# Optimization experiments

Hardware: AMD Instinct MI355X
Metric: run time of the kernel (lower is better)

The kernel has to match this reference:

```python
import jax, jax.numpy as jnp
import numpy as np

N = 50000   # nodes
E = 800000  # edges (avg in-degree 16)
H = 4       # attention heads
F = 64      # in/out feats per head
NEG_SLOPE = 0.2  # DGL GATConv default


def setup_inputs() -> dict:
    key = jax.random.key(0)
    ks = jax.random.split(key, 12)
    s = 0.1
    x = jax.random.normal(ks[0], (N, F), jnp.float32)
    src = jax.random.randint(ks[1], (E,), 0, N, jnp.int32)
    dst = jax.random.randint(ks[2], (E,), 0, N, jnp.int32)
    W1 = (jax.random.normal(ks[3], (F, H * F), jnp.float32) * s)
    al1 = (jax.random.normal(ks[4], (H, F), jnp.float32) * s)
    ar1 = (jax.random.normal(ks[5], (H, F), jnp.float32) * s)
    b1 = jnp.zeros((H, F), jnp.float32)
    W2 = (jax.random.normal(ks[6], (F, H * F), jnp.float32) * s)
    al2 = (jax.random.normal(ks[7], (H, F), jnp.float32) * s)
    ar2 = (jax.random.normal(ks[8], (H, F), jnp.float32) * s)
    b2 = jnp.zeros((H, F), jnp.float32)
    return dict(x=x, src=src, dst=dst, W1=W1, al1=al1, ar1=ar1, b1=b1,
                W2=W2, al2=al2, ar2=ar2, b2=b2)


def _gat_layer(x, src, dst, W, al, ar, b):
    # Linear projection, split into heads: [N, H, F]
    h = (x @ W).reshape(N, H, F)
    # Per-node attention logits: [N, H]
    el = jnp.einsum('nhf,hf->nh', h, al)
    er = jnp.einsum('nhf,hf->nh', h, ar)
    # Per-edge score, LeakyReLU: [E, H]
    e = jax.nn.leaky_relu(el[src] + er[dst], NEG_SLOPE)
    # Edge-softmax over incoming edges of each dst node (segment softmax)
    emax = jax.ops.segment_max(e, dst, num_segments=N)        # [N, H]
    ee = jnp.exp(e - emax[dst])                               # [E, H]
    denom = jax.ops.segment_sum(ee, dst, num_segments=N)      # [N, H]
    alpha = ee / denom[dst]                                   # [E, H]
    # Weighted aggregation: gather src feats, scale, scatter-add to dst
    m = h[src] * alpha[..., None]                              # [E, H, F]
    out = jax.ops.segment_sum(m, dst, num_segments=N)          # [N, H, F]
    return out + b[None]


def reference(x, src, dst, W1, al1, ar1, b1, W2, al2, ar2, b2):
    # Layer 1: GATConv with tanh activation, then head-mean
    h = _gat_layer(x, src, dst, W1, al1, ar1, b1)
    h = jnp.tanh(h).mean(axis=-2)              # [N, F]
    # Layer 2: GATConv (no activation), then head-mean
    h = _gat_layer(h, src, dst, W2, al2, ar2, b2)
    return h.mean(axis=-2)                     # [N, F]
```

## Files before the change

### kernel.cpp

```cpp
#include <hip/hip_runtime.h>
#include <hip/hip_fp16.h>
#include <cfloat>
#include <cstddef>

#define NODES 50000
#define EDGES 800000
#define HEADS 4
#define FEAT  64
#define HF    256
#define NEG_SLOPE 0.2f


__global__ void zero_deg_kernel(int* __restrict__ deg) {
  int i = blockIdx.x * blockDim.x + threadIdx.x;
  if (i < NODES) deg[i] = 0;
}

__global__ void count_deg_kernel(const int* __restrict__ dst, int* __restrict__ deg) {
  int e = blockIdx.x * blockDim.x + threadIdx.x;
  if (e < EDGES) atomicAdd(&deg[dst[e]], 1);
}

__global__ __launch_bounds__(1024) void scan_kernel(const int* __restrict__ deg,
                                                    int* __restrict__ rowstart,
                                                    int* __restrict__ cursor) {
  __shared__ int wtot[16], wexcl[16];
  __shared__ int carry_s;
  const int tid = threadIdx.x, lane = tid & 63, wv = tid >> 6;
  if (tid == 0) carry_s = 0;
  __syncthreads();
  for (int base = 0; base < NODES; base += 4096) {
    const int i0 = base + tid * 4;
    int v0 = (i0 + 0 < NODES) ? deg[i0 + 0] : 0;
    int v1 = (i0 + 1 < NODES) ? deg[i0 + 1] : 0;
    int v2 = (i0 + 2 < NODES) ? deg[i0 + 2] : 0;
    int v3 = (i0 + 3 < NODES) ? deg[i0 + 3] : 0;
    const int t = v0 + v1 + v2 + v3;
    int x = t;
#pragma unroll
    for (int off = 1; off < 64; off <<= 1) {
      int u = __shfl_up(x, off, 64);
      if (lane >= off) x += u;
    }
    if (lane == 63) wtot[wv] = x;
    __syncthreads();
    if (wv == 0) {
      int wval = (lane < 16) ? wtot[lane] : 0;
      int wx = wval;
#pragma unroll
      for (int off = 1; off < 16; off <<= 1) {
        int u = __shfl_up(wx, off, 64);
        if (lane >= off) wx += u;
      }
      if (lane < 16) wexcl[lane] = wx - wval;
    }
    __syncthreads();
    const int carry = carry_s;
    int e = carry + wexcl[wv] + (x - t);
    if (i0 + 0 < NODES) { rowstart[i0 + 0] = e; cursor[i0 + 0] = e; } e += v0;
    if (i0 + 1 < NODES) { rowstart[i0 + 1] = e; cursor[i0 + 1] = e; } e += v1;
    if (i0 + 2 < NODES) { rowstart[i0 + 2] = e; cursor[i0 + 2] = e; } e += v2;
    if (i0 + 3 < NODES) { rowstart[i0 + 3] = e; cursor[i0 + 3] = e; }
    __syncthreads();
    if (tid == 1023) carry_s = carry + wexcl[15] + wtot[15];
    __syncthreads();
  }
}

__global__ void scatter_kernel(const int* __restrict__ src, const int* __restrict__ dst,
                               int* __restrict__ cursor, int* __restrict__ csr_src) {
  int e = blockIdx.x * blockDim.x + threadIdx.x;
  if (e < EDGES) {
    int pos = atomicAdd(&cursor[dst[e]], 1);
    csr_src[pos] = src[e];
  }
}

template<int ROWS>
__global__ __launch_bounds__(256) void proj_kernel(
    const float* __restrict__ x, const float* __restrict__ W,
    const float* __restrict__ al, const float* __restrict__ ar,
    __half* __restrict__ h, float* __restrict__ el, float* __restrict__ er) {
  __shared__ float xs[ROWS * FEAT];
  const int c = threadIdx.x;
  const int head = c >> 6, f = c & 63;

  float Wc[FEAT];
#pragma unroll
  for (int k = 0; k < FEAT; ++k) Wc[k] = W[k * HF + c];
  const float alv = al[head * FEAT + f];
  const float arv = ar[head * FEAT + f];

  const int row0 = blockIdx.x * ROWS;
  for (int i = c; i < ROWS * FEAT; i += 256) {
    int r = row0 + (i >> 6);
    xs[i] = (r < NODES) ? x[r * FEAT + (i & 63)] : 0.f;
  }
  __syncthreads();

  for (int r = 0; r < ROWS; ++r) {
    const int row = row0 + r;
    if (row >= NODES) break;
    const float4* xr = (const float4*)&xs[r * FEAT];
    float v = 0.f;
#pragma unroll
    for (int k4 = 0; k4 < 16; ++k4) {
      float4 xv = xr[k4];
      v += xv.x * Wc[4 * k4 + 0] + xv.y * Wc[4 * k4 + 1] +
           xv.z * Wc[4 * k4 + 2] + xv.w * Wc[4 * k4 + 3];
    }
    h[(size_t)row * HF + c] = __float2half(v);
    float sl = v * alv, sr = v * arv;
#pragma unroll
    for (int m = 32; m; m >>= 1) {
      sl += __shfl_xor(sl, m, 64);
      sr += __shfl_xor(sr, m, 64);
    }
    if (f == 0) {
      el[row * HEADS + head] = sl;
      er[row * HEADS + head] = sr;
    }
  }
}

__device__ __forceinline__ float lrelu(float s) { return s > 0.f ? s : NEG_SLOPE * s; }

__device__ __forceinline__ void gather_fma(const __half* __restrict__ h, int s,
                                           int hh, int fq, float av, float4& acc) {
  union { uint2 u; __half2 h2[2]; } cvt;
  cvt.u = *(const uint2*)(h + (size_t)s * HF + hh * FEAT + fq * 4);
  float2 f01 = __half22float2(cvt.h2[0]);
  float2 f23 = __half22float2(cvt.h2[1]);
  acc.x += f01.x * av;
  acc.y += f01.y * av;
  acc.z += f23.x * av;
  acc.w += f23.y * av;
}

template<int DO_TANH>
__global__ __launch_bounds__(256) void node_kernel(
    const int* __restrict__ rowstart, const int* __restrict__ deg,
    const int* __restrict__ csr_src,
    const float* __restrict__ el, const float* __restrict__ er,
    const __half* __restrict__ h, const float* __restrict__ bias,
    float* __restrict__ out) {
  const int node = (blockIdx.x * blockDim.x + threadIdx.x) >> 6;
  if (node >= NODES) return;
  const int lane = threadIdx.x & 63;
  const int hh = lane >> 4, fq = lane & 15;
  const int rs = rowstart[node];
  const int dg = deg[node];

  float4 acc = make_float4(0.f, 0.f, 0.f, 0.f);

  if (dg > 0) {
    const float4 erv = *(const float4*)&er[node * 4];
    if (dg <= 64) {
      int sL = 0;
      float s0 = -FLT_MAX, s1 = -FLT_MAX, s2 = -FLT_MAX, s3 = -FLT_MAX;
      if (lane < dg) {
        sL = csr_src[rs + lane];
        float4 ev = *(const float4*)&el[sL * 4];
        s0 = lrelu(ev.x + erv.x);
        s1 = lrelu(ev.y + erv.y);
        s2 = lrelu(ev.z + erv.z);
        s3 = lrelu(ev.w + erv.w);
      }
      float m0 = s0, m1 = s1, m2 = s2, m3 = s3;
#pragma unroll
      for (int off = 32; off; off >>= 1) {
        m0 = fmaxf(m0, __shfl_xor(m0, off, 64));
        m1 = fmaxf(m1, __shfl_xor(m1, off, 64));
        m2 = fmaxf(m2, __shfl_xor(m2, off, 64));
        m3 = fmaxf(m3, __shfl_xor(m3, off, 64));
      }
      float E0 = 0.f, E1 = 0.f, E2 = 0.f, E3 = 0.f;
      if (lane < dg) {
        E0 = __expf(s0 - m0);
        E1 = __expf(s1 - m1);
        E2 = __expf(s2 - m2);
        E3 = __expf(s3 - m3);
      }
      float q0 = E0, q1 = E1, q2 = E2, q3 = E3;
#pragma unroll
      for (int off = 32; off; off >>= 1) {
        q0 += __shfl_xor(q0, off, 64);
        q1 += __shfl_xor(q1, off, 64);
        q2 += __shfl_xor(q2, off, 64);
        q3 += __shfl_xor(q3, off, 64);
      }
      const float A0 = E0 / q0, A1 = E1 / q1, A2 = E2 / q2, A3 = E3 / q3;
      for (int i = 0; i < dg; ++i) {
        const int s = __shfl(sL, i, 64);
        const float a0 = __shfl(A0, i, 64);
        const float a1 = __shfl(A1, i, 64);
        const float a2 = __shfl(A2, i, 64);
        const float a3 = __shfl(A3, i, 64);
        const float av = (hh == 0) ? a0 : (hh == 1) ? a1 : (hh == 2) ? a2 : a3;
        gather_fma(h, s, hh, fq, av, acc);
      }
    } else {
      float m0 = -FLT_MAX, m1 = -FLT_MAX, m2 = -FLT_MAX, m3 = -FLT_MAX;
      for (int i = lane; i < dg; i += 64) {
        int s = csr_src[rs + i];
        float4 ev = *(const float4*)&el[s * 4];
        m0 = fmaxf(m0, lrelu(ev.x + erv.x));
        m1 = fmaxf(m1, lrelu(ev.y + erv.y));
        m2 = fmaxf(m2, lrelu(ev.z + erv.z));
        m3 = fmaxf(m3, lrelu(ev.w + erv.w));
      }
#pragma unroll
      for (int off = 32; off; off >>= 1) {
        m0 = fmaxf(m0, __shfl_xor(m0, off, 64));
        m1 = fmaxf(m1, __shfl_xor(m1, off, 64));
        m2 = fmaxf(m2, __shfl_xor(m2, off, 64));
        m3 = fmaxf(m3, __shfl_xor(m3, off, 64));
      }
      float q0 = 0.f, q1 = 0.f, q2 = 0.f, q3 = 0.f;
      for (int i = lane; i < dg; i += 64) {
        int s = csr_src[rs + i];
        float4 ev = *(const float4*)&el[s * 4];
        q0 += __expf(lrelu(ev.x + erv.x) - m0);
        q1 += __expf(lrelu(ev.y + erv.y) - m1);
        q2 += __expf(lrelu(ev.z + erv.z) - m2);
        q3 += __expf(lrelu(ev.w + erv.w) - m3);
      }
#pragma unroll
      for (int off = 32; off; off >>= 1) {
        q0 += __shfl_xor(q0, off, 64);
        q1 += __shfl_xor(q1, off, 64);
        q2 += __shfl_xor(q2, off, 64);
        q3 += __shfl_xor(q3, off, 64);
      }
      const float r0 = 1.f / q0, r1 = 1.f / q1, r2 = 1.f / q2, r3 = 1.f / q3;
      for (int base = 0; base < dg; base += 64) {
        const int cnt = min(64, dg - base);
        int sL = 0;
        float A0 = 0.f, A1 = 0.f, A2 = 0.f, A3 = 0.f;
        if (base + lane < dg) {
          sL = csr_src[rs + base + lane];
          float4 ev = *(const float4*)&el[sL * 4];
          A0 = __expf(lrelu(ev.x + erv.x) - m0) * r0;
          A1 = __expf(lrelu(ev.y + erv.y) - m1) * r1;
          A2 = __expf(lrelu(ev.z + erv.z) - m2) * r2;
          A3 = __expf(lrelu(ev.w + erv.w) - m3) * r3;
        }
        for (int i = 0; i < cnt; ++i) {
          const int s = __shfl(sL, i, 64);
          const float a0 = __shfl(A0, i, 64);
          const float a1 = __shfl(A1, i, 64);
          const float a2 = __shfl(A2, i, 64);
          const float a3 = __shfl(A3, i, 64);
          const float av = (hh == 0) ? a0 : (hh == 1) ? a1 : (hh == 2) ? a2 : a3;
          gather_fma(h, s, hh, fq, av, acc);
        }
      }
    }
  }

  const float4 bv = *(const float4*)&bias[hh * FEAT + fq * 4];
  float vx = acc.x + bv.x, vy = acc.y + bv.y, vz = acc.z + bv.z, vw = acc.w + bv.w;
  if (DO_TANH) { vx = tanhf(vx); vy = tanhf(vy); vz = tanhf(vz); vw = tanhf(vw); }
#pragma unroll
  for (int off = 16; off <= 32; off <<= 1) {
    vx += __shfl_xor(vx, off, 64);
    vy += __shfl_xor(vy, off, 64);
    vz += __shfl_xor(vz, off, 64);
    vw += __shfl_xor(vw, off, 64);
  }
  if (hh == 0) {
    *(float4*)&out[(size_t)node * FEAT + fq * 4] =
        make_float4(vx * 0.25f, vy * 0.25f, vz * 0.25f, vw * 0.25f);
  }
}


extern "C" void kernel_launch(void* const* d_in, const int* in_sizes, int n_in,
                              void* d_out, int out_size, void* d_ws, size_t ws_size,
                              hipStream_t stream) {
  const float* x   = (const float*)d_in[0];
  const int*   src = (const int*)d_in[1];
  const int*   dst = (const int*)d_in[2];
  const float* Ws[2]  = {(const float*)d_in[3], (const float*)d_in[7]};
  const float* als[2] = {(const float*)d_in[4], (const float*)d_in[8]};
  const float* ars[2] = {(const float*)d_in[5], (const float*)d_in[9]};
  const float* bs[2]  = {(const float*)d_in[6], (const float*)d_in[10]};

  float* ws = (float*)d_ws;
  const size_t NHF = (size_t)NODES * HF;
  const size_t NF  = (size_t)NODES * FEAT;
  const size_t NH  = (size_t)NODES * HEADS;
  __half* hbuf = (__half*)ws;
  float* x2   = ws + NHF / 2;
  float* el   = x2 + NF;
  float* er   = el + NH;
  int* ibase   = (int*)(er + NH);
  int* deg      = ibase;
  int* rowstart = ibase + NODES;
  int* cursor   = ibase + 2 * NODES;
  int* csr_src  = ibase + 3 * NODES;
  float* outp = (float*)d_out;

  const int ROWS = 32;
  const int proj_grid = (NODES + ROWS - 1) / ROWS;
  const int edge_grid = (EDGES + 255) / 256;
  const int node_grid = (NODES * 64) / 256;
  const int n_grid    = (NODES + 255) / 256;

  zero_deg_kernel<<<n_grid, 256, 0, stream>>>(deg);
  count_deg_kernel<<<edge_grid, 256, 0, stream>>>(dst, deg);
  scan_kernel<<<1, 1024, 0, stream>>>(deg, rowstart, cursor);
  scatter_kernel<<<edge_grid, 256, 0, stream>>>(src, dst, cursor, csr_src);

  proj_kernel<ROWS><<<proj_grid, 256, 0, stream>>>(x, Ws[0], als[0], ars[0], hbuf, el, er);
  node_kernel<1><<<node_grid, 256, 0, stream>>>(rowstart, deg, csr_src, el, er,
                                                hbuf, bs[0], x2);
  proj_kernel<ROWS><<<proj_grid, 256, 0, stream>>>(x2, Ws[1], als[1], ars[1], hbuf, el, er);
  node_kernel<0><<<node_grid, 256, 0, stream>>>(rowstart, deg, csr_src, el, er,
                                                hbuf, bs[1], outp);
}
```

Before: 492.3 us.

## Fuse degree counting into layer-1 projection and stage scan through shared memory

Folds the edge in-degree atomic counting into the first projection kernel as extra blocks. This removes one launch and lets the counting overlap with the projection GEMM. The single-block scan now loads 13312-element chunks into LDS, with each thread doing a serial scan over 13 elements, which cuts the number of loop iterations and barriers. The projection dot product is also split into four independent accumulators to shorten the FMA dependency chain. The costs are a larger LDS footprint in the scan and mixed work types inside one grid.

```diff
diff --git a/kernel.cpp b/kernel.cpp
--- a/kernel.cpp
+++ b/kernel.cpp
@@ -10,59 +10,71 @@
 #define HF    256
 #define NEG_SLOPE 0.2f
 
+#define ROWS 32
+#define PROJ_BLOCKS ((NODES + ROWS - 1) / ROWS)
+#define COUNT_BLOCKS ((EDGES + 255) / 256)
+
 
 __global__ void zero_deg_kernel(int* __restrict__ deg) {
   int i = blockIdx.x * blockDim.x + threadIdx.x;
   if (i < NODES) deg[i] = 0;
 }
 
-__global__ void count_deg_kernel(const int* __restrict__ dst, int* __restrict__ deg) {
-  int e = blockIdx.x * blockDim.x + threadIdx.x;
-  if (e < EDGES) atomicAdd(&deg[dst[e]], 1);
-}
-
+#define SCHUNK 13312
+#define SPER   13
 __global__ __launch_bounds__(1024) void scan_kernel(const int* __restrict__ deg,
                                                     int* __restrict__ rowstart,
                                                     int* __restrict__ cursor) {
-  __shared__ int wtot[16], wexcl[16];
+  __shared__ int buf[SCHUNK];
+  __shared__ int wsum[16];
   __shared__ int carry_s;
   const int tid = threadIdx.x, lane = tid & 63, wv = tid >> 6;
   if (tid == 0) carry_s = 0;
-  __syncthreads();
-  for (int base = 0; base < NODES; base += 4096) {
-    const int i0 = base + tid * 4;
-    int v0 = (i0 + 0 < NODES) ? deg[i0 + 0] : 0;
-    int v1 = (i0 + 1 < NODES) ? deg[i0 + 1] : 0;
-    int v2 = (i0 + 2 < NODES) ? deg[i0 + 2] : 0;
-    int v3 = (i0 + 3 < NODES) ? deg[i0 + 3] : 0;
-    const int t = v0 + v1 + v2 + v3;
-    int x = t;
+  for (int base = 0; base < NODES; base += SCHUNK) {
+    const int sz = min(SCHUNK, NODES - base);
+    for (int i = tid; i < sz; i += 1024) buf[i] = deg[base + i];
+    __syncthreads();
+    const int o = tid * SPER;
+    int tsum = 0;
+#pragma unroll
+    for (int j = 0; j < SPER; ++j) {
+      int idx = o + j;
+      if (idx < sz) tsum += buf[idx];
+    }
+    int x = tsum;
 #pragma unroll
     for (int off = 1; off < 64; off <<= 1) {
       int u = __shfl_up(x, off, 64);
       if (lane >= off) x += u;
     }
-    if (lane == 63) wtot[wv] = x;
+    if (lane == 63) wsum[wv] = x;
     __syncthreads();
     if (wv == 0) {
-      int wval = (lane < 16) ? wtot[lane] : 0;
+      int wval = (lane < 16) ? wsum[lane] : 0;
       int wx = wval;
 #pragma unroll
       for (int off = 1; off < 16; off <<= 1) {
         int u = __shfl_up(wx, off, 64);
         if (lane >= off) wx += u;
       }
-      if (lane < 16) wexcl[lane] = wx - wval;
+      if (lane < 16) wsum[lane] = wx - wval;
     }
     __syncthreads();
     const int carry = carry_s;
-    int e = carry + wexcl[wv] + (x - t);
-    if (i0 + 0 < NODES) { rowstart[i0 + 0] = e; cursor[i0 + 0] = e; } e += v0;
-    if (i0 + 1 < NODES) { rowstart[i0 + 1] = e; cursor[i0 + 1] = e; } e += v1;
-    if (i0 + 2 < NODES) { rowstart[i0 + 2] = e; cursor[i0 + 2] = e; } e += v2;
-    if (i0 + 3 < NODES) { rowstart[i0 + 3] = e; cursor[i0 + 3] = e; }
-    __syncthreads();
-    if (tid == 1023) carry_s = carry + wexcl[15] + wtot[15];
+    int run = carry + wsum[wv] + (x - tsum);
+#pragma unroll
+    for (int j = 0; j < SPER; ++j) {
+      int idx = o + j;
+      if (idx < sz) { int t = buf[idx]; buf[idx] = run; run += t; }
+    }
+    __syncthreads();
+    for (int i = tid; i < sz; i += 1024) {
+      int v = buf[i];
+      rowstart[base + i] = v;
+      cursor[base + i] = v;
+    }
+    __syncthreads();
+    if (tid == 1023) carry_s = run;
     __syncthreads();
   }
 }
@@ -76,11 +88,11 @@
   }
 }
 
-template<int ROWS>
-__global__ __launch_bounds__(256) void proj_kernel(
+__device__ __forceinline__ void proj_body(
     const float* __restrict__ x, const float* __restrict__ W,
     const float* __restrict__ al, const float* __restrict__ ar,
-    __half* __restrict__ h, float* __restrict__ el, float* __restrict__ er) {
+    __half* __restrict__ h, float* __restrict__ el, float* __restrict__ er,
+    int blk) {
   __shared__ float xs[ROWS * FEAT];
   const int c = threadIdx.x;
   const int head = c >> 6, f = c & 63;
@@ -91,7 +103,7 @@
   const float alv = al[head * FEAT + f];
   const float arv = ar[head * FEAT + f];
 
-  const int row0 = blockIdx.x * ROWS;
+  const int row0 = blk * ROWS;
   for (int i = c; i < ROWS * FEAT; i += 256) {
     int r = row0 + (i >> 6);
     xs[i] = (r < NODES) ? x[r * FEAT + (i & 63)] : 0.f;
@@ -102,13 +114,23 @@
     const int row = row0 + r;
     if (row >= NODES) break;
     const float4* xr = (const float4*)&xs[r * FEAT];
-    float v = 0.f;
-#pragma unroll
-    for (int k4 = 0; k4 < 16; ++k4) {
-      float4 xv = xr[k4];
-      v += xv.x * Wc[4 * k4 + 0] + xv.y * Wc[4 * k4 + 1] +
-           xv.z * Wc[4 * k4 + 2] + xv.w * Wc[4 * k4 + 3];
-    }
+    float vs0 = 0.f, vs1 = 0.f, vs2 = 0.f, vs3 = 0.f;
+#pragma unroll
+    for (int k4 = 0; k4 < 16; k4 += 4) {
+      float4 a = xr[k4 + 0];
+      float4 b = xr[k4 + 1];
+      float4 cc = xr[k4 + 2];
+      float4 d = xr[k4 + 3];
+      vs0 += a.x * Wc[4 * k4 + 0] + a.y * Wc[4 * k4 + 1] +
+             a.z * Wc[4 * k4 + 2] + a.w * Wc[4 * k4 + 3];
+      vs1 += b.x * Wc[4 * k4 + 4] + b.y * Wc[4 * k4 + 5] +
+             b.z * Wc[4 * k4 + 6] + b.w * Wc[4 * k4 + 7];
+      vs2 += cc.x * Wc[4 * k4 + 8] + cc.y * Wc[4 * k4 + 9] +
+             cc.z * Wc[4 * k4 + 10] + cc.w * Wc[4 * k4 + 11];
+      vs3 += d.x * Wc[4 * k4 + 12] + d.y * Wc[4 * k4 + 13] +
+             d.z * Wc[4 * k4 + 14] + d.w * Wc[4 * k4 + 15];
+    }
+    const float v = (vs0 + vs1) + (vs2 + vs3);
     h[(size_t)row * HF + c] = __float2half(v);
     float sl = v * alv, sr = v * arv;
 #pragma unroll
@@ -121,6 +143,20 @@
       er[row * HEADS + head] = sr;
     }
   }
+}
+
+template<int WITH_COUNT>
+__global__ __launch_bounds__(256) void proj_kernel(
+    const float* __restrict__ x, const float* __restrict__ W,
+    const float* __restrict__ al, const float* __restrict__ ar,
+    __half* __restrict__ h, float* __restrict__ el, float* __restrict__ er,
+    const int* __restrict__ dst, int* __restrict__ deg) {
+  if (WITH_COUNT && blockIdx.x >= PROJ_BLOCKS) {
+    int e = (blockIdx.x - PROJ_BLOCKS) * 256 + threadIdx.x;
+    if (e < EDGES) atomicAdd(&deg[dst[e]], 1);
+    return;
+  }
+  proj_body(x, W, al, ar, h, el, er, blockIdx.x);
 }
 
 __device__ __forceinline__ float lrelu(float s) { return s > 0.f ? s : NEG_SLOPE * s; }
@@ -301,21 +337,20 @@
   int* csr_src  = ibase + 3 * NODES;
   float* outp = (float*)d_out;
 
-  const int ROWS = 32;
-  const int proj_grid = (NODES + ROWS - 1) / ROWS;
   const int edge_grid = (EDGES + 255) / 256;
   const int node_grid = (NODES * 64) / 256;
   const int n_grid    = (NODES + 255) / 256;
 
   zero_deg_kernel<<<n_grid, 256, 0, stream>>>(deg);
-  count_deg_kernel<<<edge_grid, 256, 0, stream>>>(dst, deg);
+  proj_kernel<1><<<PROJ_BLOCKS + COUNT_BLOCKS, 256, 0, stream>>>(
+      x, Ws[0], als[0], ars[0], hbuf, el, er, dst, deg);
   scan_kernel<<<1, 1024, 0, stream>>>(deg, rowstart, cursor);
   scatter_kernel<<<edge_grid, 256, 0, stream>>>(src, dst, cursor, csr_src);
 
-  proj_kernel<ROWS><<<proj_grid, 256, 0, stream>>>(x, Ws[0], als[0], ars[0], hbuf, el, er);
   node_kernel<1><<<node_grid, 256, 0, stream>>>(rowstart, deg, csr_src, el, er,
                                                 hbuf, bs[0], x2);
-  proj_kernel<ROWS><<<proj_grid, 256, 0, stream>>>(x2, Ws[1], als[1], ars[1], hbuf, el, er);
+  proj_kernel<0><<<PROJ_BLOCKS, 256, 0, stream>>>(
+      x2, Ws[1], als[1], ars[1], hbuf, el, er, dst, deg);
   node_kernel<0><<<node_grid, 256, 0, stream>>>(rowstart, deg, csr_src, el, er,
                                                 hbuf, bs[1], outp);
 }
```

Measured after the change: 464.4 us. 5.7% less time.
